# Optimization experiments

Hardware: AMD Instinct MI355X
Metric: run time of the kernel (lower is better)

Reference implementation:

```python
import jax, jax.numpy as jnp
import numpy as np
import math

NUM_TOKENS = 8192
MODEL_DIM = 2048
NUM_EXPERTS = 64
CAPACITY_FACTOR = 1.0


def setup_inputs() -> dict:
    key = jax.random.key(0)
    k1, k2 = jax.random.split(key)
    x = jax.random.normal(k1, (NUM_TOKENS, MODEL_DIM), dtype=jnp.float32)
    # gate weight: nn.Linear(model_dim, num_experts, bias=False) -> [E, D]
    wg = jax.random.normal(k2, (NUM_EXPERTS, MODEL_DIM), dtype=jnp.float32) * (1.0 / math.sqrt(MODEL_DIM))
    return {"x": x, "wg": wg}


def reference(x, wg):
    num_tokens, _ = x.shape
    num_experts = wg.shape[0]
    # training mode: capacity = capacity_factor * ceil(tokens / experts)
    capacity = int(CAPACITY_FACTOR * math.ceil(num_tokens / num_experts))

    logits = x @ wg.T                                   # [S, E]
    gates = jax.nn.softmax(logits, axis=1)              # [S, E]

    indices1_s = jnp.argmax(gates, axis=1)              # [S] top-1 expert
    mask1 = jax.nn.one_hot(indices1_s, num_experts, dtype=gates.dtype)  # [S, E]

    gates1_s = jnp.sum(gates * mask1, axis=1)           # [S] top-1 gate value

    # fused_cumsum_sub_one: position of each token within its expert queue
    locations1 = jnp.cumsum(mask1.astype(jnp.int32), axis=0) - 1        # [S, E]

    # load-balancing aux loss
    me = jnp.mean(gates, axis=0)                        # [E]
    ce = jnp.mean(mask1, axis=0)                        # [E]
    l_aux = jnp.mean(me * ce) * (num_experts * num_experts)

    # drop tokens beyond expert capacity
    mask1 = mask1 * (locations1 < capacity).astype(mask1.dtype)         # [S, E]
    locations1_s = jnp.sum(locations1 * mask1.astype(jnp.int32), axis=1)  # [S]

    gates1 = gates1_s[:, None] * mask1                  # [S, E]
    locations1_sc = jax.nn.one_hot(locations1_s, capacity, dtype=gates.dtype)  # [S, C]

    # combine[s, e, c] = gates1[s, e] * onehot_loc[s, c]  (bmm of rank-1 outer products)
    combine1_sec = gates1[:, :, None] * locations1_sc[:, None, :]       # [S, E, C]
    dispatch_mask = combine1_sec.astype(bool)
    return (l_aux, combine1_sec, dispatch_mask)
```

## Files before the change

### kernel.cpp

```cpp
#include <hip/hip_runtime.h>
#include <hip/hip_bf16.h>

#define S_TOK    8192
#define D_DIM    2048
#define N_EXP    64
#define CAPACITY 128
#define SEC      ((size_t)S_TOK * N_EXP * CAPACITY)

#define KS2   4
#define KR2   (D_DIM / KS2)
#define BT    64
#define BK    64
#define LSTR  68

__global__ __launch_bounds__(256, 2) void k1a_gemm(const float* __restrict__ x,
                                                   const float* __restrict__ wg,
                                                   float* __restrict__ part) {
    __shared__ __align__(16) float Xs[BT * LSTR];
    __shared__ __align__(16) float Ws[BK * LSTR];

    const int tid   = threadIdx.x;
    const int blk   = blockIdx.x;
    const int split = blk & (KS2 - 1);
    const int tB    = (blk >> 2) * BT;

    const int tx = tid & 15, ty = tid >> 4;
    const int e0 = tx * 4,   t0 = ty * 4;

    const int lcol = tid & 15;
    const int lrow = tid >> 4;

    float acc[4][4] = {};

    const float* xbase = x  + (size_t)tB * D_DIM + split * KR2 + 4 * lcol;
    const float* wbase = wg + split * KR2 + 4 * lcol;

    float4 gx[4], gw[4];
#pragma unroll
    for (int j = 0; j < 4; ++j) {
        gx[j] = *(const float4*)(xbase + (size_t)(lrow + 16 * j) * D_DIM);
        gw[j] = *(const float4*)(wbase + (size_t)(lrow + 16 * j) * D_DIM);
    }

#pragma unroll 1
    for (int kt = 0; kt < KR2; kt += BK) {
#pragma unroll
        for (int j = 0; j < 4; ++j) {
            *(float4*)&Xs[(lrow + 16 * j) * LSTR + 4 * lcol] = gx[j];
            const int e = lrow + 16 * j;
            Ws[(4 * lcol + 0) * LSTR + e] = gw[j].x;
            Ws[(4 * lcol + 1) * LSTR + e] = gw[j].y;
            Ws[(4 * lcol + 2) * LSTR + e] = gw[j].z;
            Ws[(4 * lcol + 3) * LSTR + e] = gw[j].w;
        }
        __syncthreads();

        if (kt + BK < KR2) {
#pragma unroll
            for (int j = 0; j < 4; ++j) {
                gx[j] = *(const float4*)(xbase + (size_t)(lrow + 16 * j) * D_DIM + kt + BK);
                gw[j] = *(const float4*)(wbase + (size_t)(lrow + 16 * j) * D_DIM + kt + BK);
            }
        }

#pragma unroll
        for (int kk = 0; kk < BK; kk += 4) {
            float av[4][4];
            float bv[4][4];
#pragma unroll
            for (int tt = 0; tt < 4; ++tt)
                *(float4*)av[tt] = *(const float4*)&Xs[(t0 + tt) * LSTR + kk];
#pragma unroll
            for (int ki = 0; ki < 4; ++ki)
                *(float4*)bv[ki] = *(const float4*)&Ws[(kk + ki) * LSTR + e0];
#pragma unroll
            for (int tt = 0; tt < 4; ++tt)
#pragma unroll
                for (int ee = 0; ee < 4; ++ee) {
                    float a = acc[tt][ee];
                    a = fmaf(av[tt][0], bv[0][ee], a);
                    a = fmaf(av[tt][1], bv[1][ee], a);
                    a = fmaf(av[tt][2], bv[2][ee], a);
                    a = fmaf(av[tt][3], bv[3][ee], a);
                    acc[tt][ee] = a;
                }
        }
        __syncthreads();
    }

#pragma unroll
    for (int tt = 0; tt < 4; ++tt) {
        float* prow = part + ((size_t)split * S_TOK + tB + t0 + tt) * N_EXP + e0;
        *(float4*)prow = make_float4(acc[tt][0], acc[tt][1], acc[tt][2], acc[tt][3]);
    }
}

__global__ __launch_bounds__(64) void k1b_softmax(const float* __restrict__ part,
                                                  int*   __restrict__ idxArr,
                                                  float* __restrict__ gateArr,
                                                  float* __restrict__ mep) {
    const int lane  = threadIdx.x;
    const int token = blockIdx.x * 64 + lane;

    float l[N_EXP];
    {
        const float* p0 = part + (size_t)token * N_EXP;
#pragma unroll
        for (int i = 0; i < 16; ++i) ((float4*)l)[i] = ((const float4*)p0)[i];
    }
#pragma unroll 1
    for (int sp = 1; sp < KS2; ++sp) {
        const float* ps = part + ((size_t)sp * S_TOK + token) * N_EXP;
#pragma unroll
        for (int i = 0; i < 16; ++i) {
            float4 v = ((const float4*)ps)[i];
            float4* a = ((float4*)l) + i;
            a->x += v.x; a->y += v.y; a->z += v.z; a->w += v.w;
        }
    }

    float best = l[0];
    int   bi   = 0;
#pragma unroll
    for (int e = 1; e < N_EXP; ++e) {
        if (l[e] > best) { best = l[e]; bi = e; }
    }

    float sum = 0.0f;
#pragma unroll
    for (int e = 0; e < N_EXP; ++e) sum += __expf(l[e] - best);
    const float inv = 1.0f / sum;

    idxArr[token]  = bi;
    gateArr[token] = inv;

#pragma unroll 1
    for (int e = 0; e < N_EXP; ++e) {
        float v = __expf(l[e] - best) * inv;
#pragma unroll
        for (int off = 32; off > 0; off >>= 1) v += __shfl_xor(v, off, 64);
        if (lane == 0) mep[(size_t)blockIdx.x * N_EXP + e] = v;
    }
}

__global__ __launch_bounds__(1024) void k2_scan(const int*   __restrict__ idxArr,
                                                const float* __restrict__ mep,
                                                const float* __restrict__ gateArr,
                                                float* __restrict__ out) {
    __shared__ int   hist[16][N_EXP];
    __shared__ int   cbase[16][N_EXP];
    __shared__ int   totalSm[N_EXP];
    __shared__ float mered[8][N_EXP];

    const int tid  = threadIdx.x;
    const int lane = tid & 63;
    const int w    = tid >> 6;

    int eTok[8];

    int cnt = 0;
#pragma unroll 1
    for (int g = 0; g < 8; ++g) {
        const int s = w * 512 + g * 64 + lane;
        const int e = idxArr[s];
        eTok[g] = e;
        unsigned long long bal[6];
#pragma unroll
        for (int b = 0; b < 6; ++b) bal[b] = __ballot((e >> b) & 1);
        unsigned long long mE = ~0ull;
#pragma unroll
        for (int b = 0; b < 6; ++b) mE &= ((lane >> b) & 1) ? bal[b] : ~bal[b];
        cnt += __popcll(mE);
    }
    hist[w][lane] = cnt;
    __syncthreads();

    if (tid < 64) {
        int run = 0;
#pragma unroll 1
        for (int w2 = 0; w2 < 16; ++w2) {
            cbase[w2][tid] = run;
            run += hist[w2][tid];
        }
        totalSm[tid] = run;
    }
    if (tid >= 64 && tid < 576) {
        const int t2 = tid - 64;
        const int e  = t2 & 63;
        const int h  = t2 >> 6;
        float sacc = 0.0f;
#pragma unroll 1
        for (int p = h * 16; p < h * 16 + 16; ++p) sacc += mep[(size_t)p * N_EXP + e];
        mered[h][e] = sacc;
    }
    __syncthreads();

    int runB = 0;
#pragma unroll 1
    for (int g = 0; g < 8; ++g) {
        const int e = eTok[g];
        unsigned long long bal[6];
#pragma unroll
        for (int b = 0; b < 6; ++b) bal[b] = __ballot((e >> b) & 1);
        unsigned long long mE = ~0ull, mT = ~0ull;
#pragma unroll
        for (int b = 0; b < 6; ++b) {
            const unsigned long long bb = bal[b];
            mE &= ((lane >> b) & 1) ? bb : ~bb;
            mT &= ((e    >> b) & 1) ? bb : ~bb;
        }
        const unsigned long long below = (1ull << lane) - 1ull;
        const int rank = __popcll(mT & below);
        const int base = cbase[w][e];
        const int runE = __shfl(runB, e, 64);
        const int pos  = base + runE + rank;
        const int s    = w * 512 + g * 64 + lane;
        if (pos < CAPACITY) {
            const size_t off = 1 + (size_t)s * (N_EXP * CAPACITY)
                             + (size_t)e * CAPACITY + pos;
            out[off]       = gateArr[s];
            out[off + SEC] = 1.0f;
        }
        runB += __popcll(mE);
    }

    if (tid < 64) {
        float me = 0.0f;
#pragma unroll
        for (int h = 0; h < 8; ++h) me += mered[h][tid];
        me *= (1.0f / (float)S_TOK);
        const float ce = (float)totalSm[tid] * (1.0f / (float)S_TOK);
        float v = me * ce;
#pragma unroll
        for (int off = 32; off > 0; off >>= 1) v += __shfl_xor(v, off, 64);
        if (tid == 0) out[0] = v * 64.0f;
    }
}

extern "C" void kernel_launch(void* const* d_in, const int* in_sizes, int n_in,
                              void* d_out, int out_size, void* d_ws, size_t ws_size,
                              hipStream_t stream) {
    const float* x  = (const float*)d_in[0];
    const float* wg = (const float*)d_in[1];
    float* out = (float*)d_out;

    char* ws = (char*)d_ws;
    const size_t partBytes = (size_t)KS2 * S_TOK * N_EXP * 4;
    float* part    = (float*)ws;
    int*   idxArr  = (int*)  (ws + partBytes);
    float* gateArr = (float*)(ws + partBytes + S_TOK * 4);
    float* mep     = (float*)(ws + partBytes + S_TOK * 8);

    hipMemsetAsync((char*)d_out + 4, 0, ((size_t)out_size - 1) * sizeof(float), stream);

    k1a_gemm   <<<(S_TOK / BT) * KS2, 256,  0, stream>>>(x, wg, part);
    k1b_softmax<<<S_TOK / 64,         64,   0, stream>>>(part, idxArr, gateArr, mep);
    k2_scan    <<<1,                  1024, 0, stream>>>(idxArr, mep, gateArr, out);
}
```

Baseline: 674.3 us.

## Fuse output zero-fill into GEMM kernel to overlap memset with compute

Replaces the separate hipMemsetAsync of the large output with extra blocks in the GEMM launch that write zeros with float4 stores, interleaving two fill blocks per GEMM block so the bandwidth-bound fill overlaps the compute-bound GEMM. It also drops the register prefetch double-buffering in the GEMM loop in favour of load-then-sync, which may expose global load latency. The fill covers 1024*32768 float4s starting at out[0], which includes the l_aux slot later written by k2, plus one trailing float.

```diff
diff --git a/kernel.cpp b/kernel.cpp
--- a/kernel.cpp
+++ b/kernel.cpp
@@ -13,14 +13,33 @@
 #define BK    64
 #define LSTR  68
 
-__global__ __launch_bounds__(256, 2) void k1a_gemm(const float* __restrict__ x,
-                                                   const float* __restrict__ wg,
-                                                   float* __restrict__ part) {
+#define NGEMM  (S_TOK / BT * KS2)
+#define NFILL  1024
+#define F4_PER_BLK 32768
+
+__global__ __launch_bounds__(256, 2) void k1_fill_gemm(const float* __restrict__ x,
+                                                       const float* __restrict__ wg,
+                                                       float* __restrict__ part,
+                                                       float* __restrict__ out) {
     __shared__ __align__(16) float Xs[BT * LSTR];
     __shared__ __align__(16) float Ws[BK * LSTR];
 
-    const int tid   = threadIdx.x;
-    const int blk   = blockIdx.x;
+    const int tid = threadIdx.x;
+    const int b   = blockIdx.x;
+
+    if (b % 3 != 0) {
+        const int fid = (b / 3) * 2 + (b % 3) - 1;
+        float4* o4 = (float4*)out;
+        const size_t base = (size_t)fid * F4_PER_BLK + tid;
+        const float4 z = make_float4(0.f, 0.f, 0.f, 0.f);
+#pragma unroll 8
+        for (int i = 0; i < F4_PER_BLK / 256; ++i)
+            o4[base + (size_t)i * 256] = z;
+        if (fid == 0 && tid == 0) out[2 * SEC] = 0.0f;
+        return;
+    }
+
+    const int blk   = b / 3;
     const int split = blk & (KS2 - 1);
     const int tB    = (blk >> 2) * BT;
 
@@ -35,15 +54,15 @@
     const float* xbase = x  + (size_t)tB * D_DIM + split * KR2 + 4 * lcol;
     const float* wbase = wg + split * KR2 + 4 * lcol;
 
-    float4 gx[4], gw[4];
-#pragma unroll
-    for (int j = 0; j < 4; ++j) {
-        gx[j] = *(const float4*)(xbase + (size_t)(lrow + 16 * j) * D_DIM);
-        gw[j] = *(const float4*)(wbase + (size_t)(lrow + 16 * j) * D_DIM);
-    }
-
 #pragma unroll 1
     for (int kt = 0; kt < KR2; kt += BK) {
+        float4 gx[4], gw[4];
+#pragma unroll
+        for (int j = 0; j < 4; ++j) {
+            gx[j] = *(const float4*)(xbase + (size_t)(lrow + 16 * j) * D_DIM + kt);
+            gw[j] = *(const float4*)(wbase + (size_t)(lrow + 16 * j) * D_DIM + kt);
+        }
+        __syncthreads();
 #pragma unroll
         for (int j = 0; j < 4; ++j) {
             *(float4*)&Xs[(lrow + 16 * j) * LSTR + 4 * lcol] = gx[j];
@@ -54,14 +73,6 @@
             Ws[(4 * lcol + 3) * LSTR + e] = gw[j].w;
         }
         __syncthreads();
-
-        if (kt + BK < KR2) {
-#pragma unroll
-            for (int j = 0; j < 4; ++j) {
-                gx[j] = *(const float4*)(xbase + (size_t)(lrow + 16 * j) * D_DIM + kt + BK);
-                gw[j] = *(const float4*)(wbase + (size_t)(lrow + 16 * j) * D_DIM + kt + BK);
-            }
-        }
 
 #pragma unroll
         for (int kk = 0; kk < BK; kk += 4) {
@@ -85,7 +96,6 @@
                     acc[tt][ee] = a;
                 }
         }
-        __syncthreads();
     }
 
 #pragma unroll
@@ -251,9 +261,7 @@
     float* gateArr = (float*)(ws + partBytes + S_TOK * 4);
     float* mep     = (float*)(ws + partBytes + S_TOK * 8);
 
-    hipMemsetAsync((char*)d_out + 4, 0, ((size_t)out_size - 1) * sizeof(float), stream);
-
-    k1a_gemm   <<<(S_TOK / BT) * KS2, 256,  0, stream>>>(x, wg, part);
-    k1b_softmax<<<S_TOK / 64,         64,   0, stream>>>(part, idxArr, gateArr, mep);
-    k2_scan    <<<1,                  1024, 0, stream>>>(idxArr, mep, gateArr, out);
-}
+    k1_fill_gemm<<<NGEMM + NFILL, 256,  0, stream>>>(x, wg, part, out);
+    k1b_softmax <<<S_TOK / 64,    64,   0, stream>>>(part, idxArr, gateArr, mep);
+    k2_scan     <<<1,             1024, 0, stream>>>(idxArr, mep, gateArr, out);
+}
```

Measured after the change: 665.6 us. No clear change (-1.3%).
